# Kernel optimization log

Hardware: AMD Instinct MI355X
Metric: run time of the kernel (lower is better)

## Reference

```python
import jax, jax.numpy as jnp
import numpy as np

TH = 1.0            # q_threshold for all IF neurons
POS_MAX = 7.0       # level//2 - 1, level=16, sym=True
NEG_MIN = -8.0      # -(level//2)
PREFIRE = 0.2       # attn_softmax_IF.prefire
S_QUANT = 7.0       # spiking_softmax scale = level//2 - 1
NUM_HEADS = 8


def if_step(x, vmem0, acc0, th=TH, pos_max=POS_MAX, neg_min=NEG_MIN):
    """One timestep of a symmetric ST-BIF neuron with straight-through surrogate.
    Forward: spike in {-1,0,+1}*th gated by membrane and accumulator saturation.
    Backward: identity (STE), accumulator is a constant."""
    acc0f = acc0.astype(x.dtype)
    v = vmem0 + x
    pos = jnp.logical_and(v >= th, acc0f < pos_max)
    neg = jnp.logical_and(v < 0.0, acc0f > neg_min)
    spike = pos.astype(x.dtype) - neg.astype(x.dtype)
    out_hard = spike * th
    out = x + jax.lax.stop_gradient(out_hard - x)  # STE: fwd=spike*th, bwd=identity
    acc = jax.lax.stop_gradient(acc0f + spike)     # running spike count (constant wrt grads)
    return out, acc


def setup_inputs() -> dict:
    key = jax.random.key(0)
    ks = jax.random.split(key, 16)
    B, N, C, H = 4, 1024, 512, NUM_HEADS
    D = C // H
    f32 = jnp.float32
    inp = {
        "x": jax.random.normal(ks[0], (B, N, C), dtype=f32),
        "w_qkv": jax.random.normal(ks[1], (3 * C, C), dtype=f32) * 0.02,
        "b_qkv": jnp.zeros((3 * C,), dtype=f32),
        "w_proj": jax.random.normal(ks[2], (C, C), dtype=f32) * 0.02,
        "b_proj": jnp.zeros((C,), dtype=f32),
        "q_vmem": jax.random.uniform(ks[3], (B, H, N, D), dtype=f32),
        "k_vmem": jax.random.uniform(ks[4], (B, H, N, D), dtype=f32),
        "v_vmem": jax.random.uniform(ks[5], (B, H, N, D), dtype=f32),
        "attn_vmem": jax.random.uniform(ks[6], (B, H, N, N), dtype=f32),
        "q_acc0": jax.random.randint(ks[7], (B, H, N, D), 0, 8).astype(jnp.int32),
        "k_acc0": jax.random.randint(ks[8], (B, H, N, D), 0, 8).astype(jnp.int32),
        "v_acc0": jax.random.randint(ks[9], (B, H, N, D), 0, 8).astype(jnp.int32),
        "attn_acc0": jax.random.randint(ks[10], (B, H, N, N), 0, 8).astype(jnp.int32),
    }
    return inp


def reference(x, w_qkv, b_qkv, w_proj, b_proj,
              q_vmem, k_vmem, v_vmem, attn_vmem,
              q_acc0, k_acc0, v_acc0, attn_acc0):
    B, N, C = x.shape
    H = NUM_HEADS
    D = C // H
    scale = D ** -0.5
    sg = jax.lax.stop_gradient

    # qkv projection -> [3, B, H, N, D]
    qkv = (x @ w_qkv.T + b_qkv).reshape(B, N, 3, H, D).transpose(2, 0, 3, 1, 4)
    q_in, k_in, v_in = qkv[0], qkv[1], qkv[2]

    # ST-BIF IF neurons (one timestep, carried state)
    q_s, q_acc = if_step(q_in, q_vmem, q_acc0)
    k_s, k_acc = if_step(k_in, k_vmem, k_acc0)
    v_s, v_acc = if_step(v_in, v_vmem, v_acc0)

    q = q_s * scale
    # accumulator corrections: acc_q * q_threshold (*scale for q) minus detached spike output
    q_corr = sg(q_acc * TH * scale - q)
    k_corr = sg(k_acc * TH - k_s)
    v_corr = sg(v_acc * TH - v_s)

    # multi: (q + q_corr) @ k^T + q @ k_corr^T   -> [B, H, N, N]
    attn = (jnp.einsum('bhnd,bhmd->bhnm', q + q_corr, k_s)
            + jnp.einsum('bhnd,bhmd->bhnm', q, k_corr))

    # spiking softmax substitute: softmax of the (accumulated) scores, scaled to quant range
    attn = jax.nn.softmax(attn, axis=-1) * S_QUANT

    # attn_softmax_IF with prefire bias on the membrane
    attn_s, attn_acc = if_step(attn, attn_vmem + PREFIRE * TH, attn_acc0)
    attn_corr = sg(attn_acc * TH - attn_s)

    # multi1: (attn + attn_corr) @ v + attn @ v_corr  -> [B, H, N, D]
    out = (jnp.einsum('bhnm,bhmd->bhnd', attn_s + attn_corr, v_s)
           + jnp.einsum('bhnm,bhmd->bhnd', attn_s, v_corr))

    # after_attn_IF: fresh state (rounding init 0.5*th, zero accumulator)
    out, _ = if_step(out, jnp.asarray(0.5 * TH, out.dtype), jnp.zeros_like(out))

    out = out.transpose(0, 2, 1, 3).reshape(B, N, C)
    return out @ w_proj.T + b_proj
```

## Files before the change

kernel.cpp:

```cpp
#include <hip/hip_runtime.h>
#include <hip/hip_bf16.h>
#include <cstdint>

typedef short short8 __attribute__((ext_vector_type(8)));
typedef float f32x4 __attribute__((ext_vector_type(4)));
typedef int   int4v __attribute__((ext_vector_type(4)));
typedef _Float16 fp16x8 __attribute__((ext_vector_type(8)));

using bf16 = __hip_bfloat16;

#define MFMA16(a, b, c) __builtin_amdgcn_mfma_f32_16x16x32_bf16((a), (b), (c), 0, 0, 0)
#define MFMAI8(a, b, c) __builtin_amdgcn_mfma_i32_16x16x64_i8((a), (b), (c), 0, 0, 0)
#define MFMAF16(a, b, c) __builtin_amdgcn_mfma_f32_16x16x32_f16((a), (b), (c), 0, 0, 0)

__device__ __forceinline__ short8 ldb8(const bf16* p) {
    return *reinterpret_cast<const short8*>(p);
}
__device__ __forceinline__ int lo16(unsigned u) { return (int)(u << 16) >> 16; }
__device__ __forceinline__ int hi16(unsigned u) { return (int)u >> 16; }

__global__ __launch_bounds__(256) void k_prep(
    const float* __restrict__ X, const float* __restrict__ W, const float* __restrict__ Wp,
    _Float16* __restrict__ Xh, _Float16* __restrict__ Xl,
    _Float16* __restrict__ Wh, _Float16* __restrict__ Wl, bf16* __restrict__ Wpb)
{
    const int NX = 4096 * 512, NW = 1536 * 512, NP = 512 * 512;
    for (int i = blockIdx.x * 256 + threadIdx.x; i < NX + NW + NP; i += gridDim.x * 256) {
        if (i < NX) {
            const float v = X[i] * 512.0f;
            const _Float16 h = (_Float16)v;
            Xh[i] = h;
            Xl[i] = (_Float16)((v - (float)h) * 2048.0f);
        } else if (i < NX + NW) {
            const int j = i - NX;
            const float v = W[j] * 512.0f;
            const _Float16 h = (_Float16)v;
            Wh[j] = h;
            Wl[j] = (_Float16)((v - (float)h) * 2048.0f);
        } else {
            const int j = i - NX - NW;
            Wpb[j] = __float2bfloat16(Wp[j]);
        }
    }
}

__global__ __launch_bounds__(256, 3) void k_qkv_f16(
    const _Float16* __restrict__ Xh, const _Float16* __restrict__ Xl,
    const _Float16* __restrict__ Wh, const _Float16* __restrict__ Wl,
    const float* __restrict__ bq,
    const float* __restrict__ qvm, const float* __restrict__ kvm, const float* __restrict__ vvm,
    const int* __restrict__ qac, const int* __restrict__ kac, const int* __restrict__ vac,
    int8_t* __restrict__ Q2, int8_t* __restrict__ K2c,
    int8_t* __restrict__ VsT, int8_t* __restrict__ VaT)
{
    const int tid = threadIdx.x;
    const int w = tid >> 6, lane = tid & 63, lo = lane & 15, hi = lane >> 4;
    const int wr = w >> 1, wc = w & 1;
    const int r0 = blockIdx.y * 64 + wr * 32;
    const int c0 = blockIdx.x * 128 + wc * 64;

    f32x4 hh[2][4] = {};
    f32x4 md[2][4] = {};

    const _Float16* xhp = Xh + (size_t)(r0 + lo) * 512 + hi * 8;
    const _Float16* xlp = Xl + (size_t)(r0 + lo) * 512 + hi * 8;
    const _Float16* whp = Wh + (size_t)(c0 + lo) * 512 + hi * 8;
    const _Float16* wlp = Wl + (size_t)(c0 + lo) * 512 + hi * 8;

    for (int kc = 0; kc < 16; ++kc) {
        const int ko = kc * 32;
        const fp16x8 Ah0 = *reinterpret_cast<const fp16x8*>(xhp + ko);
        const fp16x8 Ah1 = *reinterpret_cast<const fp16x8*>(xhp + ko + 16 * 512);
        const fp16x8 Al0 = *reinterpret_cast<const fp16x8*>(xlp + ko);
        const fp16x8 Al1 = *reinterpret_cast<const fp16x8*>(xlp + ko + 16 * 512);
        fp16x8 Bh[4], Bl[4];
        #pragma unroll
        for (int j = 0; j < 4; ++j) {
            Bh[j] = *reinterpret_cast<const fp16x8*>(whp + ko + j * 16 * 512);
            Bl[j] = *reinterpret_cast<const fp16x8*>(wlp + ko + j * 16 * 512);
        }
        #pragma unroll
        for (int j = 0; j < 4; ++j) {
            hh[0][j] = MFMAF16(Ah0, Bh[j], hh[0][j]);
            hh[1][j] = MFMAF16(Ah1, Bh[j], hh[1][j]);
            md[0][j] = MFMAF16(Ah0, Bl[j], md[0][j]);
            md[0][j] = MFMAF16(Al0, Bh[j], md[0][j]);
            md[1][j] = MFMAF16(Ah1, Bl[j], md[1][j]);
            md[1][j] = MFMAF16(Al1, Bh[j], md[1][j]);
        }
    }

    const int sel = (unsigned)c0 >> 9;
    const float* VM = (sel == 0) ? qvm : (sel == 1) ? kvm : vvm;
    const int*   AC = (sel == 0) ? qac : (sel == 1) ? kac : vac;

    #pragma unroll
    for (int i = 0; i < 2; ++i) {
        const int rowb = r0 + i * 16 + hi * 4;
        const int b = rowb >> 10, nb = rowb & 1023;
        #pragma unroll
        for (int j = 0; j < 4; ++j) {
            const int c = c0 + j * 16 + lo;
            const int ch = c & 511;
            const int hh_ = ch >> 6, d = ch & 63;
            const int bh = b * 8 + hh_;
            const float bcol = bq[c];
            int sp[4], a4[4];
            #pragma unroll
            for (int r = 0; r < 4; ++r) {
                const size_t gi = (size_t)(bh * 1024 + nb + r) * 64 + d;
                const float vm = VM[gi];
                const int a0 = AC[gi];
                const float val = fmaf(md[i][j][r], 0x1p-11f, hh[i][j][r]) * 0x1p-18f;
                const float v_ = vm + (val + bcol);
                int s = ((v_ >= 1.0f) && (a0 < 7)) ? 1 : 0;
                if (v_ < 0.0f) s -= 1;
                sp[r] = s; a4[r] = a0;
            }
            if (sel == 2) {
                uchar4 us, ua;
                us.x = (uint8_t)sp[0]; us.y = (uint8_t)sp[1]; us.z = (uint8_t)sp[2]; us.w = (uint8_t)sp[3];
                ua.x = (uint8_t)(a4[0] + sp[0]); ua.y = (uint8_t)(a4[1] + sp[1]);
                ua.z = (uint8_t)(a4[2] + sp[2]); ua.w = (uint8_t)(a4[3] + sp[3]);
                const size_t vi = (size_t)(bh * 64 + d) * 1024 + nb;
                *reinterpret_cast<uchar4*>(VsT + vi) = us;
                *reinterpret_cast<uchar4*>(VaT + vi) = ua;
            } else {
                int8_t* base = ((sel == 0) ? Q2 : K2c) + (size_t)(bh * 1024 + nb) * 128 + d;
                #pragma unroll
                for (int r = 0; r < 4; ++r) {
                    const int v0 = (sel == 0) ? a4[r] + sp[r] : sp[r];
                    const int v1 = (sel == 0) ? sp[r]         : a4[r];
                    base[r * 128]      = (int8_t)v0;
                    base[r * 128 + 64] = (int8_t)v1;
                }
            }
        }
    }
}

__global__ __launch_bounds__(256, 4) void k_av0(
    const int* __restrict__ aac, const int8_t* __restrict__ VsT,
    uint8_t* __restrict__ aac8, int* __restrict__ AV0)
{
    const int w = threadIdx.x >> 6, lane = threadIdx.x & 63;
    const int lo = lane & 15, hi = lane >> 4;
    const int bh = blockIdx.y;
    const int hk = blockIdx.z;
    const int ko0 = hk * 512;
    const int row = blockIdx.x * 64 + w * 16 + lo;
    const size_t arow = ((size_t)bh * 1024 + row) * 1024;

    int4 buf[2][4];
    {
        const int4* ap0 = reinterpret_cast<const int4*>(aac + arow + ko0 + hi * 16);
        const int4* ap1 = reinterpret_cast<const int4*>(aac + arow + ko0 + 64 + hi * 16);
        #pragma unroll
        for (int j = 0; j < 4; ++j) { buf[0][j] = ap0[j]; buf[1][j] = ap1[j]; }
    }

    int4v acc[4] = {{0,0,0,0},{0,0,0,0},{0,0,0,0},{0,0,0,0}};
    #pragma unroll
    for (int tt = 0; tt < 8; ++tt) {
        int4 c[4];
        #pragma unroll
        for (int j = 0; j < 4; ++j) c[j] = buf[tt & 1][j];
        if (tt < 6) {
            const int4* ap = reinterpret_cast<const int4*>(aac + arow + ko0 + (tt + 2) * 64 + hi * 16);
            #pragma unroll
            for (int j = 0; j < 4; ++j) buf[tt & 1][j] = ap[j];
        }
        int4v af;
        af[0] = (int)(unsigned)(c[0].x | (c[0].y << 8) | (c[0].z << 16) | (c[0].w << 24));
        af[1] = (int)(unsigned)(c[1].x | (c[1].y << 8) | (c[1].z << 16) | (c[1].w << 24));
        af[2] = (int)(unsigned)(c[2].x | (c[2].y << 8) | (c[2].z << 16) | (c[2].w << 24));
        af[3] = (int)(unsigned)(c[3].x | (c[3].y << 8) | (c[3].z << 16) | (c[3].w << 24));
        *reinterpret_cast<int4v*>(aac8 + arow + ko0 + tt * 64 + hi * 16) = af;
        #pragma unroll
        for (int dt = 0; dt < 4; ++dt) {
            const int4v bf = *reinterpret_cast<const int4v*>(
                VsT + ((size_t)(bh * 64 + dt * 16 + lo)) * 1024 + ko0 + tt * 64 + hi * 16);
            acc[dt] = MFMAI8(af, bf, acc[dt]);
        }
    }
    int* outp = AV0 + (size_t)hk * 32 * 1024 * 64;
    #pragma unroll
    for (int dt = 0; dt < 4; ++dt)
        #pragma unroll
        for (int r = 0; r < 4; ++r)
            outp[((size_t)bh * 1024 + blockIdx.x * 64 + w * 16 + hi * 4 + r) * 64 + dt * 16 + lo] = acc[dt][r];
}

__global__ __launch_bounds__(256, 4) void k_attn(
    const int8_t* __restrict__ Q2, const int8_t* __restrict__ K2c,
    const float* __restrict__ avm, const uint8_t* __restrict__ aac8,
    const int8_t* __restrict__ Vsum, const int* __restrict__ AV0,
    bf16* __restrict__ O2)
{
    __shared__ alignas(16) char Sc[16896];
    int*   const maxb = (int*)(Sc + 16384);
    float* const sumb = (float*)(Sc + 16640);
    const int w = threadIdx.x >> 6, lane = threadIdx.x & 63;
    const int lo = lane & 15, hi = lane >> 4;
    const int bh = blockIdx.z * 8 + blockIdx.y;
    const int n0 = blockIdx.x * 16;

    unsigned pA[16][2];
    {
        const int8_t* qb = Q2 + ((size_t)(bh * 1024 + n0 + lo)) * 128 + hi * 16;
        const int4v qa0 = *reinterpret_cast<const int4v*>(qb);
        const int4v qa1 = *reinterpret_cast<const int4v*>(qb + 64);
        const int8_t* kbp = K2c + ((size_t)(bh * 1024 + w * 256 + lo)) * 128 + hi * 16;
        int4v b0[2], b1[2];
        b0[0] = *reinterpret_cast<const int4v*>(kbp);
        b1[0] = *reinterpret_cast<const int4v*>(kbp + 64);
        b0[1] = *reinterpret_cast<const int4v*>(kbp + 2048);
        b1[1] = *reinterpret_cast<const int4v*>(kbp + 2048 + 64);
        #pragma unroll
        for (int t = 0; t < 16; ++t) {
            const int4v c0f = b0[t & 1], c1f = b1[t & 1];
            if (t < 14) {
                const int8_t* np = kbp + (t + 2) * 2048;
                b0[t & 1] = *reinterpret_cast<const int4v*>(np);
                b1[t & 1] = *reinterpret_cast<const int4v*>(np + 64);
            }
            int4v s = {0, 0, 0, 0};
            s = MFMAI8(c0f, qa0, s);
            s = MFMAI8(c1f, qa1, s);
            pA[t][0] = (s[0] & 0xFFFF) | ((unsigned)s[1] << 16);
            pA[t][1] = (s[2] & 0xFFFF) | ((unsigned)s[3] << 16);
        }
    }

    const float*   vmp = avm  + ((size_t)(bh * 1024 + n0 + lo)) * 1024 + w * 256 + hi * 4;
    const uint8_t* acp = aac8 + ((size_t)(bh * 1024 + n0 + lo)) * 1024 + w * 256 + hi * 4;
    float4 vmr[4]; uchar4 acr[4];
#define PF(u) { vmr[(u)&3] = *reinterpret_cast<const float4*>(vmp + (u)*16); \
                acr[(u)&3] = *reinterpret_cast<const uchar4*>(acp + (u)*16); }
    PF(0) PF(1) PF(2) PF(3)

    int mxi = -32768;
    #pragma unroll
    for (int t = 0; t < 16; ++t) {
        mxi = max(mxi, max(max(lo16(pA[t][0]), hi16(pA[t][0])),
                           max(lo16(pA[t][1]), hi16(pA[t][1]))));
    }
    mxi = max(mxi, __shfl_xor(mxi, 16));
    mxi = max(mxi, __shfl_xor(mxi, 32));
    if (lane < 16) maxb[w * 16 + lo] = mxi;
    __syncthreads();
    const int M = max(max(maxb[lo], maxb[16 + lo]), max(maxb[32 + lo], maxb[48 + lo]));

    const float kls = 0.18033688011112042f;
    float sum = 0.f;
    #pragma unroll
    for (int t = 0; t < 16; ++t) {
        sum += exp2f(kls * (float)(lo16(pA[t][0]) - M));
        sum += exp2f(kls * (float)(hi16(pA[t][0]) - M));
        sum += exp2f(kls * (float)(lo16(pA[t][1]) - M));
        sum += exp2f(kls * (float)(hi16(pA[t][1]) - M));
    }
    sum += __shfl_xor(sum, 16);
    sum += __shfl_xor(sum, 32);
    if (lane < 16) sumb[w * 16 + lo] = sum;
    __syncthreads();
    const float rsum = 7.0f / ((sumb[lo] + sumb[16 + lo]) + (sumb[32 + lo] + sumb[48 + lo]));

    #pragma unroll
    for (int u = 0; u < 16; ++u) {
        const float4 vm = vmr[u & 3];
        const uchar4 a8 = acr[u & 3];
        if (u < 12) PF(u + 4)
        const int sv[4] = { lo16(pA[u][0]), hi16(pA[u][0]), lo16(pA[u][1]), hi16(pA[u][1]) };
        const float vr[4] = { vm.x, vm.y, vm.z, vm.w };
        const int   ar[4] = { a8.x, a8.y, a8.z, a8.w };
        unsigned pk = 0;
        #pragma unroll
        for (int i = 0; i < 4; ++i) {
            const float e_ = exp2f(kls * (float)(sv[i] - M));
            const float p7 = e_ * rsum;
            const float v_ = (vr[i] + 0.2f) + p7;
            const unsigned sp = ((v_ >= 1.0f) && (ar[i] < 7)) ? 1u : 0u;
            pk |= sp << (8 * i);
        }
        char* pb = Sc + lo * 1024 + ((w * 256 + u * 16 + hi * 4) ^ ((lo & 7) << 4));
        *reinterpret_cast<unsigned*>(pb) = pk;
    }
#undef PF
    __syncthreads();

    {
        const int d0 = w * 16;
        const int* avp = AV0 + ((size_t)(bh * 1024 + n0 + hi * 4)) * 64 + d0 + lo;
        int av[4];
        #pragma unroll
        for (int r = 0; r < 4; ++r)
            av[r] = avp[(size_t)r * 64] + avp[(size_t)r * 64 + (size_t)32 * 1024 * 64];

        const int8_t* vp = Vsum + ((size_t)(bh * 64 + d0 + lo)) * 1024 + hi * 16;
        int4v nv0 = *reinterpret_cast<const int4v*>(vp);
        int4v nv1 = *reinterpret_cast<const int4v*>(vp + 64);
        int4v acc = {0, 0, 0, 0};
        #pragma unroll
        for (int tt = 0; tt < 16; ++tt) {
            const int4v cv = (tt & 1) ? nv1 : nv0;
            if (tt < 14) {
                if (tt & 1) nv1 = *reinterpret_cast<const int4v*>(vp + (tt + 2) * 64);
                else        nv0 = *reinterpret_cast<const int4v*>(vp + (tt + 2) * 64);
            }
            const int ko = tt * 64 + hi * 16;
            const int4v a1 = *reinterpret_cast<const int4v*>(Sc + lo * 1024 + (ko ^ ((lo & 7) << 4)));
            acc = MFMAI8(a1, cv, acc);
        }
        #pragma unroll
        for (int r = 0; r < 4; ++r) {
            const int o = acc[r] + av[r];
            const float f = (float)o;
            const float o2 = (f >= 0.5f ? 1.f : 0.f) - (f < -0.5f ? 1.f : 0.f);
            const int n = n0 + hi * 4 + r;
            O2[((size_t)(blockIdx.z * 1024 + n)) * 512 + blockIdx.y * 64 + d0 + lo] = __float2bfloat16(o2);
        }
    }
}

__global__ __launch_bounds__(256) void k_proj(
    const bf16* __restrict__ O2, const bf16* __restrict__ W, const float* __restrict__ bias,
    float* __restrict__ Y)
{
    const int w = threadIdx.x >> 6, lane = threadIdx.x & 63;
    const int lo = lane & 15, hi = lane >> 4;
    const int r0 = blockIdx.y * 16;
    const int c0 = blockIdx.x * 256 + w * 64;

    f32x4 acc[4] = {{0.f,0.f,0.f,0.f},{0.f,0.f,0.f,0.f},{0.f,0.f,0.f,0.f},{0.f,0.f,0.f,0.f}};
    const bf16* op = O2 + (size_t)(r0 + lo) * 512 + hi * 8;
    #pragma unroll 4
    for (int kb = 0; kb < 16; ++kb) {
        short8 a = ldb8(op + kb * 32);
        #pragma unroll
        for (int t = 0; t < 4; ++t) {
            short8 b = ldb8(W + (size_t)(c0 + t * 16 + lo) * 512 + kb * 32 + hi * 8);
            acc[t] = MFMA16(a, b, acc[t]);
        }
    }
    #pragma unroll
    for (int t = 0; t < 4; ++t) {
        const int col = c0 + t * 16 + lo;
        const float bcol = bias[col];
        #pragma unroll
        for (int r = 0; r < 4; ++r) {
            const int rr = r0 + hi * 4 + r;
            Y[(size_t)rr * 512 + col] = acc[t][r] + bcol;
        }
    }
}

extern "C" void kernel_launch(void* const* d_in, const int* in_sizes, int n_in,
                              void* d_out, int out_size, void* d_ws, size_t ws_size,
                              hipStream_t stream)
{
    const float* x     = (const float*)d_in[0];
    const float* wqkv  = (const float*)d_in[1];
    const float* bqkv  = (const float*)d_in[2];
    const float* wproj = (const float*)d_in[3];
    const float* bproj = (const float*)d_in[4];
    const float* qvm   = (const float*)d_in[5];
    const float* kvm   = (const float*)d_in[6];
    const float* vvm   = (const float*)d_in[7];
    const float* avm   = (const float*)d_in[8];
    const int*   qac   = (const int*)d_in[9];
    const int*   kac   = (const int*)d_in[10];
    const int*   vac   = (const int*)d_in[11];
    const int*   aac   = (const int*)d_in[12];

    char* p = (char*)d_ws;
    int8_t*   Q2   = (int8_t*)p;   p += (size_t)32 * 1024 * 128;
    int8_t*   K2c  = (int8_t*)p;   p += (size_t)32 * 1024 * 128;
    int8_t*   VsT  = (int8_t*)p;   p += (size_t)32 * 64 * 1024;
    int8_t*   VaT  = (int8_t*)p;   p += (size_t)32 * 64 * 1024;
    bf16*     O2   = (bf16*)p;     p += (size_t)4096 * 512 * 2;
    bf16*     Wpb  = (bf16*)p;     p += (size_t)512 * 512 * 2;
    _Float16* Xh   = (_Float16*)p; p += (size_t)4096 * 512 * 2;
    _Float16* Xl   = (_Float16*)p; p += (size_t)4096 * 512 * 2;
    _Float16* Wh   = (_Float16*)p; p += (size_t)1536 * 512 * 2;
    _Float16* Wl   = (_Float16*)p; p += (size_t)1536 * 512 * 2;
    uint8_t*  aac8 = (uint8_t*)p;  p += (size_t)32 * 1024 * 1024;
    int*      AV0  = (int*)p;      p += (size_t)2 * 32 * 1024 * 64 * 4;

    k_prep<<<dim3(2048), 256, 0, stream>>>(x, wqkv, wproj, Xh, Xl, Wh, Wl, Wpb);
    k_qkv_f16<<<dim3(12, 64), 256, 0, stream>>>(Xh, Xl, Wh, Wl, bqkv, qvm, kvm, vvm,
                                                qac, kac, vac, Q2, K2c, VsT, VaT);
    k_av0<<<dim3(16, 32, 2), 256, 0, stream>>>(aac, VsT, aac8, AV0);
    k_attn<<<dim3(64, 8, 4), 256, 0, stream>>>(Q2, K2c, avm, aac8, VaT, AV0, O2);
    k_proj<<<dim3(2, 256), 256, 0, stream>>>(O2, Wpb, bproj, (float*)d_out);
}
```

Measured before the change: 499.0 us.

## Stage QKV GEMM tiles through LDS with register prefetch; double-buffer proj loads

The QKV projection kernel now loads each 64x32 X tile and 128x32 W tile (high and low fp16 halves) cooperatively into shared memory. The next k-chunk is prefetched into registers while the current one is consumed, so operands are read from global memory once per block instead of once per wave. The output projection kernel gets a register double-buffer so the next k-step's loads are issued before the current MFMAs. This adds LDS use and two barriers per k-step, which may reduce occupancy and add sync cost.

```diff
diff --git a/kernel.cpp b/kernel.cpp
--- a/kernel.cpp
+++ b/kernel.cpp
@@ -53,31 +53,60 @@
     int8_t* __restrict__ Q2, int8_t* __restrict__ K2c,
     int8_t* __restrict__ VsT, int8_t* __restrict__ VaT)
 {
+    __shared__ alignas(16) _Float16 XhL[64 * 32];
+    __shared__ alignas(16) _Float16 XlL[64 * 32];
+    __shared__ alignas(16) _Float16 WhL[128 * 32];
+    __shared__ alignas(16) _Float16 WlL[128 * 32];
+
     const int tid = threadIdx.x;
     const int w = tid >> 6, lane = tid & 63, lo = lane & 15, hi = lane >> 4;
     const int wr = w >> 1, wc = w & 1;
-    const int r0 = blockIdx.y * 64 + wr * 32;
-    const int c0 = blockIdx.x * 128 + wc * 64;
+    const int r0w = blockIdx.y * 64 + wr * 32;
+    const int c0w = blockIdx.x * 128 + wc * 64;
+
+    const int srow = tid >> 2, sk8 = tid & 3;
+    const _Float16* gxh  = Xh + (size_t)(blockIdx.y * 64 + srow) * 512 + sk8 * 8;
+    const _Float16* gxl  = Xl + (size_t)(blockIdx.y * 64 + srow) * 512 + sk8 * 8;
+    const _Float16* gw0h = Wh + (size_t)(blockIdx.x * 128 + srow) * 512 + sk8 * 8;
+    const _Float16* gw1h = Wh + (size_t)(blockIdx.x * 128 + 64 + srow) * 512 + sk8 * 8;
+    const _Float16* gw0l = Wl + (size_t)(blockIdx.x * 128 + srow) * 512 + sk8 * 8;
+    const _Float16* gw1l = Wl + (size_t)(blockIdx.x * 128 + 64 + srow) * 512 + sk8 * 8;
+
+    float4 sxh, sxl, sw0h, sw1h, sw0l, sw1l;
+#define QISSUE(kc) { const int off_ = (kc) * 32; \
+    sxh  = *reinterpret_cast<const float4*>(gxh  + off_); \
+    sxl  = *reinterpret_cast<const float4*>(gxl  + off_); \
+    sw0h = *reinterpret_cast<const float4*>(gw0h + off_); \
+    sw1h = *reinterpret_cast<const float4*>(gw1h + off_); \
+    sw0l = *reinterpret_cast<const float4*>(gw0l + off_); \
+    sw1l = *reinterpret_cast<const float4*>(gw1l + off_); }
+
+    QISSUE(0)
 
     f32x4 hh[2][4] = {};
     f32x4 md[2][4] = {};
 
-    const _Float16* xhp = Xh + (size_t)(r0 + lo) * 512 + hi * 8;
-    const _Float16* xlp = Xl + (size_t)(r0 + lo) * 512 + hi * 8;
-    const _Float16* whp = Wh + (size_t)(c0 + lo) * 512 + hi * 8;
-    const _Float16* wlp = Wl + (size_t)(c0 + lo) * 512 + hi * 8;
-
     for (int kc = 0; kc < 16; ++kc) {
-        const int ko = kc * 32;
-        const fp16x8 Ah0 = *reinterpret_cast<const fp16x8*>(xhp + ko);
-        const fp16x8 Ah1 = *reinterpret_cast<const fp16x8*>(xhp + ko + 16 * 512);
-        const fp16x8 Al0 = *reinterpret_cast<const fp16x8*>(xlp + ko);
-        const fp16x8 Al1 = *reinterpret_cast<const fp16x8*>(xlp + ko + 16 * 512);
+        __syncthreads();
+        *reinterpret_cast<float4*>(XhL + tid * 8)         = sxh;
+        *reinterpret_cast<float4*>(XlL + tid * 8)         = sxl;
+        *reinterpret_cast<float4*>(WhL + tid * 8)         = sw0h;
+        *reinterpret_cast<float4*>(WhL + (tid + 256) * 8) = sw1h;
+        *reinterpret_cast<float4*>(WlL + tid * 8)         = sw0l;
+        *reinterpret_cast<float4*>(WlL + (tid + 256) * 8) = sw1l;
+        if (kc < 15) QISSUE(kc + 1);
+        __syncthreads();
+
+        const fp16x8 Ah0 = *reinterpret_cast<const fp16x8*>(XhL + (wr * 32 + lo) * 32 + hi * 8);
+        const fp16x8 Ah1 = *reinterpret_cast<const fp16x8*>(XhL + (wr * 32 + 16 + lo) * 32 + hi * 8);
+        const fp16x8 Al0 = *reinterpret_cast<const fp16x8*>(XlL + (wr * 32 + lo) * 32 + hi * 8);
+        const fp16x8 Al1 = *reinterpret_cast<const fp16x8*>(XlL + (wr * 32 + 16 + lo) * 32 + hi * 8);
         fp16x8 Bh[4], Bl[4];
         #pragma unroll
         for (int j = 0; j < 4; ++j) {
-            Bh[j] = *reinterpret_cast<const fp16x8*>(whp + ko + j * 16 * 512);
-            Bl[j] = *reinterpret_cast<const fp16x8*>(wlp + ko + j * 16 * 512);
+            const int cl = (wc * 64 + j * 16 + lo) * 32 + hi * 8;
+            Bh[j] = *reinterpret_cast<const fp16x8*>(WhL + cl);
+            Bl[j] = *reinterpret_cast<const fp16x8*>(WlL + cl);
         }
         #pragma unroll
         for (int j = 0; j < 4; ++j) {
@@ -89,18 +118,19 @@
             md[1][j] = MFMAF16(Al1, Bh[j], md[1][j]);
         }
     }
-
-    const int sel = (unsigned)c0 >> 9;
+#undef QISSUE
+
+    const int sel = (unsigned)c0w >> 9;
     const float* VM = (sel == 0) ? qvm : (sel == 1) ? kvm : vvm;
     const int*   AC = (sel == 0) ? qac : (sel == 1) ? kac : vac;
 
     #pragma unroll
     for (int i = 0; i < 2; ++i) {
-        const int rowb = r0 + i * 16 + hi * 4;
+        const int rowb = r0w + i * 16 + hi * 4;
         const int b = rowb >> 10, nb = rowb & 1023;
         #pragma unroll
         for (int j = 0; j < 4; ++j) {
-            const int c = c0 + j * 16 + lo;
+            const int c = c0w + j * 16 + lo;
             const int ch = c & 511;
             const int hh_ = ch >> 6, d = ch & 63;
             const int bh = b * 8 + hh_;
@@ -333,15 +363,26 @@
     const int c0 = blockIdx.x * 256 + w * 64;
 
     f32x4 acc[4] = {{0.f,0.f,0.f,0.f},{0.f,0.f,0.f,0.f},{0.f,0.f,0.f,0.f},{0.f,0.f,0.f,0.f}};
-    const bf16* op = O2 + (size_t)(r0 + lo) * 512 + hi * 8;
-    #pragma unroll 4
+    const bf16* op  = O2 + (size_t)(r0 + lo) * 512 + hi * 8;
+    const bf16* wp0 = W + (size_t)(c0 + lo) * 512 + hi * 8;
+
+    short8 a2[2], b2[2][4];
+    a2[0] = ldb8(op);
+    #pragma unroll
+    for (int t = 0; t < 4; ++t) b2[0][t] = ldb8(wp0 + t * 16 * 512);
+
+    #pragma unroll
     for (int kb = 0; kb < 16; ++kb) {
-        short8 a = ldb8(op + kb * 32);
-        #pragma unroll
-        for (int t = 0; t < 4; ++t) {
-            short8 b = ldb8(W + (size_t)(c0 + t * 16 + lo) * 512 + kb * 32 + hi * 8);
-            acc[t] = MFMA16(a, b, acc[t]);
-        }
+        const int cur = kb & 1, nxt = cur ^ 1;
+        if (kb < 15) {
+            a2[nxt] = ldb8(op + (kb + 1) * 32);
+            #pragma unroll
+            for (int t = 0; t < 4; ++t)
+                b2[nxt][t] = ldb8(wp0 + t * 16 * 512 + (kb + 1) * 32);
+        }
+        #pragma unroll
+        for (int t = 0; t < 4; ++t)
+            acc[t] = MFMA16(a2[cur], b2[cur][t], acc[t]);
     }
     #pragma unroll
     for (int t = 0; t < 4; ++t) {
```

Result: faster. 456.0 us (-8.6%).
